# Performance work log

Hardware: AMD Instinct MI355X
Metric: run time of the kernel (lower is better)

The kernel has to match this reference:

```python
import jax, jax.numpy as jnp
import numpy as np

B, L, H, V = 8, 512, 256, 32000
ALPHA = 0.95  # EMA coefficient from __init__
LN_EPS = 1e-5
NORM_EPS = 1e-12  # F.normalize eps


def setup_inputs() -> dict:
    key = jax.random.key(0)
    ks = jax.random.split(key, 8)
    g = lambda k, shape, scale: (jax.random.normal(k, shape, jnp.float32) * scale)
    return {
        "seq": jax.random.randint(ks[0], (B, L), 0, V),
        "embed": g(ks[1], (V, H), 0.02),
        "W1": g(ks[2], (H, 2 * H), 1.0 / np.sqrt(H)),
        "b1": jnp.zeros((2 * H,), jnp.float32),
        "W2": g(ks[3], (2 * H, H), 1.0 / np.sqrt(2 * H)),
        "b2": jnp.zeros((H,), jnp.float32),
        "gamma": jnp.ones((H,), jnp.float32),
        "beta": jnp.zeros((H,), jnp.float32),
        "Wrp": g(ks[4], (H, H), 1.0 / np.sqrt(H)),
        "brp": jnp.zeros((H,), jnp.float32),
        "Wout": g(ks[5], (H, V), 1.0 / np.sqrt(H)),
        "bout": jnp.zeros((V,), jnp.float32),
    }


def _encoder(seq, embed, W1, b1, W2, b2, gamma, beta):
    h = embed[seq]  # [B, L, H]
    ff = jnp.maximum(h @ W1 + b1, 0.0) @ W2 + b2  # Linear-ReLU-Linear
    x = h + ff
    mu = x.mean(-1, keepdims=True)
    var = ((x - mu) ** 2).mean(-1, keepdims=True)
    return (x - mu) / jnp.sqrt(var + LN_EPS) * gamma + beta  # LayerNorm


def reference(seq, embed, W1, b1, W2, b2, gamma, beta, Wrp, brp, Wout, bout):
    h = _encoder(seq, embed, W1, b1, W2, b2, gamma, beta)  # [B, L, H]
    b, l, hd = h.shape
    keys = jnp.swapaxes(h[:, :-1, :], 0, 1)  # time-major [L-1, B, H]

    def step(M, k):
        kn = k / jnp.maximum(jnp.linalg.norm(k, axis=-1, keepdims=True), NORM_EPS)
        dv = k - jnp.einsum('bij,bj->bi', M, kn)  # delta: v - M k_hat
        M = M + (1.0 - ALPHA) * jnp.einsum('bi,bj->bij', dv, kn)  # rank-1 update
        return M, None

    M0 = jnp.zeros((b, hd, hd), h.dtype)
    M, _ = jax.lax.scan(step, M0, keys)  # sequential delta-rule recurrence
    m = jnp.einsum('bij,bj->bi', M, h[:, -1, :])  # read-out with last token
    return (m @ Wrp + brp) @ Wout + bout  # [B, V]
```

## Files before the change

kernel.cpp:

```cpp
#include <hip/hip_runtime.h>

constexpr int Bz  = 8;
constexpr int Lz  = 512;
constexpr int Hz  = 256;
constexpr int H2z = 512;
constexpr int Vz  = 32000;
constexpr int Mz  = Bz * Lz;
constexpr float CF = 0.05f;
constexpr int NB  = 16;

typedef __attribute__((ext_vector_type(8))) short bfrag8;
typedef __attribute__((ext_vector_type(4))) float f32x4v;
typedef __attribute__((ext_vector_type(4))) short s4v;

static __device__ __forceinline__ short f2bf(float f) {
  unsigned u = __builtin_bit_cast(unsigned, f);
  u += 0x7fffu + ((u >> 16) & 1u);
  return (short)(u >> 16);
}

static __device__ __forceinline__ void wcvt_tile(
    const float* __restrict__ src, short* __restrict__ dst,
    int K, int N, int n0, int k0, int tid)
{
  __shared__ float tile[64][68];
  const int rr = tid >> 4, c4 = (tid & 15) << 2;
#pragma unroll
  for (int q = 0; q < 4; ++q) {
    const int kr = rr + q * 16;
    *(float4*)&tile[kr][c4] = *(const float4*)(src + (long)(k0 + kr) * N + n0 + c4);
  }
  __syncthreads();
#pragma unroll
  for (int q = 0; q < 4; ++q) {
    const int nr = rr + q * 16;
    s4v o = { f2bf(tile[c4 + 0][nr]), f2bf(tile[c4 + 1][nr]),
              f2bf(tile[c4 + 2][nr]), f2bf(tile[c4 + 3][nr]) };
    *(s4v*)(dst + (long)(n0 + nr) * K + k0 + c4) = o;
  }
}

__global__ __launch_bounds__(256) void k_wcvt2(
    const float* __restrict__ W1, const float* __restrict__ W2,
    short* __restrict__ Wt1, short* __restrict__ Wt2)
{
  const int bx = blockIdx.x, tid = threadIdx.x;
  if (bx < 32) {
    wcvt_tile(W1, Wt1, Hz, H2z, (bx & 7) * 64, (bx >> 3) * 64, tid);
  } else {
    const int b2 = bx - 32;
    wcvt_tile(W2, Wt2, H2z, Hz, (b2 & 3) * 64, (b2 >> 2) * 64, tid);
  }
}

__global__ __launch_bounds__(256) void k_mfma1(
    const int* __restrict__ seq, const float* __restrict__ embed,
    const short* __restrict__ Wt1, const float* __restrict__ b1,
    short* __restrict__ y1bf)
{
  __shared__ short As[64][32];
  __shared__ short Bs[64][32];
  const int tid = threadIdx.x;
  const int n0 = blockIdx.x * 64, m0 = blockIdx.y * 64;
  const int w = tid >> 6, l = tid & 63;
  const int srow = tid >> 2, skq = (tid & 3) << 3;
  const long abase = (long)seq[m0 + srow] * Hz;
  const f32x4v zero = {0.f, 0.f, 0.f, 0.f};
  f32x4v acc[4] = {zero, zero, zero, zero};
  for (int kc = 0; kc < Hz; kc += 32) {
    const float4 a0 = *(const float4*)(embed + abase + kc + skq);
    const float4 a1 = *(const float4*)(embed + abase + kc + skq + 4);
    const bfrag8 bvl = *(const bfrag8*)(Wt1 + (long)(n0 + srow) * Hz + kc + skq);
    __syncthreads();
    bfrag8 av = { f2bf(a0.x), f2bf(a0.y), f2bf(a0.z), f2bf(a0.w),
                  f2bf(a1.x), f2bf(a1.y), f2bf(a1.z), f2bf(a1.w) };
    *(bfrag8*)&As[srow][skq] = av;
    *(bfrag8*)&Bs[srow][skq] = bvl;
    __syncthreads();
    const bfrag8 a = *(const bfrag8*)&As[(w << 4) + (l & 15)][(l >> 4) << 3];
#pragma unroll
    for (int nn = 0; nn < 4; ++nn) {
      const bfrag8 bb = *(const bfrag8*)&Bs[(nn << 4) + (l & 15)][(l >> 4) << 3];
      acc[nn] = __builtin_amdgcn_mfma_f32_16x16x32_bf16(a, bb, acc[nn], 0, 0, 0);
    }
  }
  const int col0 = l & 15, quad = l >> 4;
#pragma unroll
  for (int nn = 0; nn < 4; ++nn) {
    const int col = n0 + (nn << 4) + col0;
    const float bias = b1[col];
#pragma unroll
    for (int i = 0; i < 4; ++i) {
      const int row = m0 + (w << 4) + (quad << 2) + i;
      y1bf[(long)row * H2z + col] = f2bf(fmaxf(acc[nn][i] + bias, 0.0f));
    }
  }
}

__global__ __launch_bounds__(256) void k_mfma2ln(
    const int* __restrict__ seq, const float* __restrict__ embed,
    const short* __restrict__ y1bf, const short* __restrict__ Wt2,
    const float* __restrict__ b2, const float* __restrict__ gamma,
    const float* __restrict__ beta, float* __restrict__ h,
    float* __restrict__ hn, short* __restrict__ Knb)
{
  __shared__ short As[16][32];
  __shared__ short Bs[256][32];
  __shared__ float red[4][16][2];
  __shared__ float red2[4][16];
  const int tid = threadIdx.x;
  const int m0 = blockIdx.x * 16;
  const int w = tid >> 6, l = tid & 63;
  const int srow = tid >> 2, skq = (tid & 3) << 3;
  const f32x4v zero = {0.f, 0.f, 0.f, 0.f};
  f32x4v acc[4] = {zero, zero, zero, zero};

  for (int kc = 0; kc < H2z; kc += 32) {
    bfrag8 av = {};
    if (tid < 64)
      av = *(const bfrag8*)(y1bf + (long)(m0 + (tid >> 2)) * H2z + kc + skq);
    bfrag8 bv[4];
#pragma unroll
    for (int q = 0; q < 4; ++q)
      bv[q] = *(const bfrag8*)(Wt2 + (long)(srow + (q << 6)) * H2z + kc + skq);
    __syncthreads();
    if (tid < 64) *(bfrag8*)&As[tid >> 2][skq] = av;
#pragma unroll
    for (int q = 0; q < 4; ++q)
      *(bfrag8*)&Bs[srow + (q << 6)][skq] = bv[q];
    __syncthreads();
    const bfrag8 a = *(const bfrag8*)&As[l & 15][(l >> 4) << 3];
#pragma unroll
    for (int nn = 0; nn < 4; ++nn) {
      const bfrag8 bb = *(const bfrag8*)&Bs[(w << 6) + (nn << 4) + (l & 15)][(l >> 4) << 3];
      acc[nn] = __builtin_amdgcn_mfma_f32_16x16x32_bf16(a, bb, acc[nn], 0, 0, 0);
    }
  }

  const int col0 = l & 15, quad = l >> 4;
  float g_r[4], be_r[4], b2_r[4];
#pragma unroll
  for (int nn = 0; nn < 4; ++nn) {
    const int col = (w << 6) + (nn << 4) + col0;
    g_r[nn] = gamma[col]; be_r[nn] = beta[col]; b2_r[nn] = b2[col];
  }

  float v[4][4];
#pragma unroll
  for (int i = 0; i < 4; ++i) {
    const int lr = (quad << 2) + i;
    const int row = m0 + lr;
    const long ebase = (long)seq[row] * Hz;
    float s = 0.0f, ss = 0.0f;
#pragma unroll
    for (int nn = 0; nn < 4; ++nn) {
      const int col = (w << 6) + (nn << 4) + col0;
      const float t = acc[nn][i] + b2_r[nn] + embed[ebase + col];
      v[i][nn] = t; s += t; ss += t * t;
    }
#pragma unroll
    for (int o = 8; o >= 1; o >>= 1) { s += __shfl_xor(s, o); ss += __shfl_xor(ss, o); }
    if ((l & 15) == 0) { red[w][lr][0] = s; red[w][lr][1] = ss; }
  }
  __syncthreads();

#pragma unroll
  for (int i = 0; i < 4; ++i) {
    const int lr = (quad << 2) + i;
    const float s  = red[0][lr][0] + red[1][lr][0] + red[2][lr][0] + red[3][lr][0];
    const float ss = red[0][lr][1] + red[1][lr][1] + red[2][lr][1] + red[3][lr][1];
    const float mu   = s * (1.0f / Hz);
    const float var  = ss * (1.0f / Hz) - mu * mu;
    const float rstd = rsqrtf(var + 1e-5f);
    float hs = 0.0f;
#pragma unroll
    for (int nn = 0; nn < 4; ++nn) {
      const float hv = (v[i][nn] - mu) * rstd * g_r[nn] + be_r[nn];
      v[i][nn] = hv; hs += hv * hv;
    }
#pragma unroll
    for (int o = 8; o >= 1; o >>= 1) hs += __shfl_xor(hs, o);
    if ((l & 15) == 0) red2[w][lr] = hs;
  }
  __syncthreads();

#pragma unroll
  for (int i = 0; i < 4; ++i) {
    const int lr = (quad << 2) + i;
    const float hs = red2[0][lr] + red2[1][lr] + red2[2][lr] + red2[3][lr];
    const float inv = 1.0f / fmaxf(sqrtf(hs), 1e-12f);
    const int row = m0 + lr;
    float* hrow  = h  + (long)row * Hz;
    float* hnrow = hn + (long)row * Hz;
    const int bb_ = row >> 9, t = row & 511;
    short* kr = Knb + ((long)bb_ * 512 + (t < 511 ? 510 - t : 511)) * Hz;
#pragma unroll
    for (int nn = 0; nn < 4; ++nn) {
      const int col = (w << 6) + (nn << 4) + col0;
      const float hv = v[i][nn];
      const float nv = hv * inv;
      hrow[col]  = hv;
      hnrow[col] = nv;
      kr[col] = (t < 511) ? f2bf(nv) : (short)0;
    }
  }
}

__global__ __launch_bounds__(256) void k_gramT(
    const short* __restrict__ Knb, const float* __restrict__ h,
    const float* __restrict__ hn, float* __restrict__ G,
    float* __restrict__ Wsol, float* __restrict__ p)
{
  const int nb = blockIdx.x, mb = blockIdx.y, b = blockIdx.z;
  __shared__ short As[64][32];
  __shared__ short Bs[64][32];
  __shared__ float Gs2[2][32][33];
  __shared__ float qs[Hz];
  if (nb > mb) {
    const int idx = ((nb * (nb - 1)) >> 1) + mb;
    if (idx >= 16) return;
    const int tid = threadIdx.x;
    qs[tid] = h[((long)b * Lz + 511) * Hz + tid];
    __syncthreads();
    const int s = idx * 32 + (tid >> 3);
    const int g = tid & 7;
    float acc = 0.0f;
    if (s <= 510) {
      const float* src = hn + ((long)b * Lz + (510 - s)) * Hz + (g << 5);
#pragma unroll
      for (int q = 0; q < 8; ++q) {
        const float4 vv = *(const float4*)(src + 4 * q);
        const int c = (g << 5) + 4 * q;
        acc += vv.x * qs[c] + vv.y * qs[c + 1] + vv.z * qs[c + 2] + vv.w * qs[c + 3];
      }
    }
#pragma unroll
    for (int o = 4; o >= 1; o >>= 1) acc += __shfl_xor(acc, o);
    if (g == 0) p[(long)b * 512 + s] = acc;
    return;
  }
  const short* Kb = Knb + (long)b * 512 * Hz;
  const int tid = threadIdx.x;
  const int w = tid >> 6, l = tid & 63;
  const int srow = tid >> 2, skq = (tid & 3) << 3;
  const f32x4v zero = {0.f, 0.f, 0.f, 0.f};
  f32x4v acc[4] = {zero, zero, zero, zero};
  for (int kc = 0; kc < Hz; kc += 32) {
    __syncthreads();
    *(bfrag8*)&As[srow][skq] = *(const bfrag8*)(Kb + (long)(mb * 64 + srow) * Hz + kc + skq);
    *(bfrag8*)&Bs[srow][skq] = *(const bfrag8*)(Kb + (long)(nb * 64 + srow) * Hz + kc + skq);
    __syncthreads();
    const bfrag8 a = *(const bfrag8*)&As[(w << 4) + (l & 15)][(l >> 4) << 3];
#pragma unroll
    for (int nn = 0; nn < 4; ++nn) {
      const bfrag8 bb = *(const bfrag8*)&Bs[(nn << 4) + (l & 15)][(l >> 4) << 3];
      acc[nn] = __builtin_amdgcn_mfma_f32_16x16x32_bf16(a, bb, acc[nn], 0, 0, 0);
    }
  }
  const int col0 = l & 15, quad = l >> 4;
  float* Gb = G + (long)b * 512 * 512;
#pragma unroll
  for (int nn = 0; nn < 4; ++nn) {
    const int col = nb * 64 + (nn << 4) + col0;
#pragma unroll
    for (int i = 0; i < 4; ++i) {
      const int row = mb * 64 + (w << 4) + (quad << 2) + i;
      Gb[(long)row * 512 + col] = acc[nn][i];
    }
  }
  if (mb != nb) return;
#pragma unroll
  for (int nn = 0; nn < 4; ++nn) {
    const int lc = (nn << 4) + col0;
#pragma unroll
    for (int i = 0; i < 4; ++i) {
      const int lr = (w << 4) + (quad << 2) + i;
      if ((lr >> 5) == (lc >> 5)) Gs2[lr >> 5][lr & 31][lc & 31] = acc[nn][i];
    }
  }
  __syncthreads();
  if (w < 2 && l < 32) {
    const int c = l;
    float wv[32];
    wv[0] = (c == 0) ? 1.0f : 0.0f;
#pragma unroll
    for (int i = 1; i < 32; ++i) {
      float sum = 0.0f;
#pragma unroll
      for (int j = 0; j < i; ++j) sum = fmaf(Gs2[w][i][j], wv[j], sum);
      wv[i] = ((i == c) ? 1.0f : 0.0f) - CF * sum;
    }
    const int blk = mb * 2 + w;
    float* dst = Wsol + ((long)(b * NB + blk) << 10) + c;
#pragma unroll
    for (int i = 0; i < 32; ++i) dst[i * 32] = wv[i];
  }
}

__global__ __launch_bounds__(256) void k_solve(
    const float* __restrict__ G, const float* __restrict__ p,
    const float* __restrict__ Wsol, float* __restrict__ d_all)
{
  __shared__ float ds[512];
  __shared__ float part[32][9];
  __shared__ float rhs[32];
  const int b = blockIdx.x, tid = threadIdx.x;
  const int i = tid >> 3, g = tid & 7;
  const float* Gb = G + (long)b * 512 * 512;
  const float* pb = p + (long)b * 512;

  for (int blk = 0; blk < NB; ++blk) {
    float acc0 = 0.0f, acc1 = 0.0f;
    const float* grow = Gb + (long)(blk * 32 + i) * 512 + (g << 2);
    int bp = 0;
    for (; bp + 1 < blk; bp += 2) {
      const float4 g0 = *(const float4*)(grow + bp * 32);
      const float4 g1 = *(const float4*)(grow + bp * 32 + 32);
      const int j0 = bp * 32 + (g << 2), j1 = j0 + 32;
      acc0 += g0.x * ds[j0] + g0.y * ds[j0 + 1] + g0.z * ds[j0 + 2] + g0.w * ds[j0 + 3];
      acc1 += g1.x * ds[j1] + g1.y * ds[j1 + 1] + g1.z * ds[j1 + 2] + g1.w * ds[j1 + 3];
    }
    if (bp < blk) {
      const float4 gv = *(const float4*)(grow + bp * 32);
      const int j = bp * 32 + (g << 2);
      acc0 += gv.x * ds[j] + gv.y * ds[j + 1] + gv.z * ds[j + 2] + gv.w * ds[j + 3];
    }
    part[i][g] = acc0 + acc1;
    __syncthreads();
    if (tid < 32) {
      const float c = part[tid][0] + part[tid][1] + part[tid][2] + part[tid][3] +
                      part[tid][4] + part[tid][5] + part[tid][6] + part[tid][7];
      rhs[tid] = pb[blk * 32 + tid] - CF * c;
      const float* wrow = Wsol + ((long)(b * NB + blk) << 10) + tid * 32;
      float dv = 0.0f;
#pragma unroll
      for (int k = 0; k < 32; k += 4) {
        const float4 wv = *(const float4*)(wrow + k);
        dv += wv.x * rhs[k] + wv.y * rhs[k + 1] + wv.z * rhs[k + 2] + wv.w * rhs[k + 3];
      }
      if (blk == NB - 1 && tid == 31) dv = 0.0f;
      ds[blk * 32 + tid] = dv;
      d_all[(long)b * 512 + blk * 32 + tid] = dv;
    }
    __syncthreads();
  }
}

__global__ __launch_bounds__(256) void k_mrp(
    const float* __restrict__ h, const float* __restrict__ d_all,
    float* __restrict__ part)
{
  __shared__ float acc_s[4][Hz];
  const int c = blockIdx.x, b = blockIdx.y, tid = threadIdx.x;
  const int w = tid >> 6, lane = tid & 63;
  const float* hb = h + (long)b * Lz * Hz;
  const float* db = d_all + ((long)b << 9);
  const int t0 = c * 16;
  const int off = lane << 2;
  float4 acc = {0.f, 0.f, 0.f, 0.f};
#pragma unroll
  for (int q = 0; q < 4; ++q) {
    const int t = t0 + (q << 2) + w;
    if (t < 511) {
      const float dv = db[510 - t];
      const float4 hv = *(const float4*)(hb + (long)t * Hz + off);
      acc.x = fmaf(dv, hv.x, acc.x); acc.y = fmaf(dv, hv.y, acc.y);
      acc.z = fmaf(dv, hv.z, acc.z); acc.w = fmaf(dv, hv.w, acc.w);
    }
  }
  *(float4*)&acc_s[w][off] = acc;
  __syncthreads();
  if (tid < Hz) {
    part[((long)b * 32 + c) * Hz + tid] =
        acc_s[0][tid] + acc_s[1][tid] + acc_s[2][tid] + acc_s[3][tid];
  }
}

__global__ __launch_bounds__(256) void k_mr2(
    const float* __restrict__ part, const float* __restrict__ Wrp,
    const float* __restrict__ brp, float* __restrict__ r)
{
  __shared__ float ms[Hz];
  const int b = blockIdx.x, tid = threadIdx.x;
  float acc = 0.0f;
#pragma unroll
  for (int c = 0; c < 32; ++c) acc += part[((long)b * 32 + c) * Hz + tid];
  ms[tid] = CF * acc;
  __syncthreads();
  float racc = 0.0f;
#pragma unroll 8
  for (int e = 0; e < Hz; ++e)
    racc = fmaf(ms[e], Wrp[(long)e * Hz + tid], racc);
  r[b * Hz + tid] = racc + brp[tid];
}

__global__ __launch_bounds__(256) void k_outproj(
    const float* __restrict__ r, const float* __restrict__ Wout,
    const float* __restrict__ bout, float* __restrict__ out)
{
  __shared__ float rs[8 * Hz];
  __shared__ float part[4][8][64];
  const int tid = threadIdx.x, w = tid >> 6, lane = tid & 63;
  ((float4*)rs)[tid * 2 + 0] = ((const float4*)r)[tid * 2 + 0];
  ((float4*)rs)[tid * 2 + 1] = ((const float4*)r)[tid * 2 + 1];
  __syncthreads();
  const int col = blockIdx.x * 64 + lane;
  float acc[8] = {};
  const int i0 = w << 6;
#pragma unroll 8
  for (int ii = 0; ii < 64; ++ii) {
    const int i = i0 + ii;
    const float wv = Wout[(long)i * Vz + col];
#pragma unroll
    for (int bb = 0; bb < 8; ++bb) acc[bb] = fmaf(rs[bb * Hz + i], wv, acc[bb]);
  }
#pragma unroll
  for (int bb = 0; bb < 8; ++bb) part[w][bb][lane] = acc[bb];
  __syncthreads();
  const float bo = bout[col];
  float s0 = part[0][w][lane] + part[1][w][lane] + part[2][w][lane] + part[3][w][lane];
  out[(long)w * Vz + col] = s0 + bo;
  const int w4 = w + 4;
  float s1 = part[0][w4][lane] + part[1][w4][lane] + part[2][w4][lane] + part[3][w4][lane];
  out[(long)w4 * Vz + col] = s1 + bo;
}

extern "C" void kernel_launch(void* const* d_in, const int* in_sizes, int n_in,
                              void* d_out, int out_size, void* d_ws, size_t ws_size,
                              hipStream_t stream)
{
  const int*   seq   = (const int*)  d_in[0];
  const float* embed = (const float*)d_in[1];
  const float* W1    = (const float*)d_in[2];
  const float* b1    = (const float*)d_in[3];
  const float* W2    = (const float*)d_in[4];
  const float* b2    = (const float*)d_in[5];
  const float* gamma = (const float*)d_in[6];
  const float* beta  = (const float*)d_in[7];
  const float* Wrp   = (const float*)d_in[8];
  const float* brp   = (const float*)d_in[9];
  const float* Wout  = (const float*)d_in[10];
  const float* bout  = (const float*)d_in[11];
  float* out = (float*)d_out;

  char* ws = (char*)d_ws;
  const size_t MB = 1024u * 1024u;
  short* y1bf = (short*)(ws);
  float* Gf   = (float*)(ws);
  float* hb   = (float*)(ws + 8 * MB);
  float* hnb  = (float*)(ws + 12 * MB);
  short* Knb  = (short*)(ws + 16 * MB);
  short* Wt1  = (short*)(ws + 18 * MB);
  short* Wt2  = (short*)(ws + 18 * MB + 256 * 1024);
  float* Wsol = (float*)(ws + 18 * MB + 512 * 1024);
  float* pbuf = (float*)(ws + 19 * MB);
  float* dall = (float*)(ws + 19 * MB + 16 * 1024);
  float* prt  = (float*)(ws + 19 * MB + 32 * 1024);
  float* rb   = (float*)(ws + 19 * MB + 288 * 1024);

  k_wcvt2<<<64, 256, 0, stream>>>(W1, W2, Wt1, Wt2);
  k_mfma1<<<dim3(H2z / 64, Mz / 64), 256, 0, stream>>>(seq, embed, Wt1, b1, y1bf);
  k_mfma2ln<<<Mz / 16, 256, 0, stream>>>(seq, embed, y1bf, Wt2, b2, gamma, beta,
                                         hb, hnb, Knb);
  k_gramT<<<dim3(8, 8, Bz), 256, 0, stream>>>(Knb, hb, hnb, Gf, Wsol, pbuf);
  k_solve<<<Bz, 256, 0, stream>>>(Gf, pbuf, Wsol, dall);
  k_mrp<<<dim3(32, Bz), 256, 0, stream>>>(hb, dall, prt);
  k_mr2<<<Bz, 256, 0, stream>>>(prt, Wrp, brp, rb);
  k_outproj<<<Vz / 64, 256, 0, stream>>>(rb, Wout, bout, out);
}
```

Measured before the change: 199.7 us.

## Pre-gather bf16 embeddings and prefetch next block's G/Wsol rows in solve

Gathered embedding rows are converted to bf16 once in the weight-conversion kernel (extra 256 blocks) into a workspace buffer. k_mfma1 then reads those bf16 rows directly instead of re-gathering and converting fp32 embeddings for each of its 8 column blocks. In the sequential k_solve loop, the next block's G row tiles, Wsol rows and p values are loaded into registers before the barrier, hiding global latency on the serial critical path. This costs more registers (gbuf[15], wbuf[8]) and one extra 2 MB buffer write and read.

```diff
diff --git a/kernel.cpp b/kernel.cpp
--- a/kernel.cpp
+++ b/kernel.cpp
@@ -42,21 +42,35 @@
 
 __global__ __launch_bounds__(256) void k_wcvt2(
     const float* __restrict__ W1, const float* __restrict__ W2,
-    short* __restrict__ Wt1, short* __restrict__ Wt2)
+    const int* __restrict__ seq, const float* __restrict__ embed,
+    short* __restrict__ Wt1, short* __restrict__ Wt2, short* __restrict__ Eg)
 {
   const int bx = blockIdx.x, tid = threadIdx.x;
   if (bx < 32) {
     wcvt_tile(W1, Wt1, Hz, H2z, (bx & 7) * 64, (bx >> 3) * 64, tid);
-  } else {
+  } else if (bx < 64) {
     const int b2 = bx - 32;
     wcvt_tile(W2, Wt2, H2z, Hz, (b2 & 3) * 64, (b2 >> 2) * 64, tid);
+  } else {
+    const int row = (bx - 64) * 16 + (tid >> 4);
+    const int c0 = (tid & 15) << 4;
+    const long src = (long)seq[row] * Hz + c0;
+    const float4 v0 = *(const float4*)(embed + src);
+    const float4 v1 = *(const float4*)(embed + src + 4);
+    const float4 v2 = *(const float4*)(embed + src + 8);
+    const float4 v3 = *(const float4*)(embed + src + 12);
+    bfrag8 o0 = { f2bf(v0.x), f2bf(v0.y), f2bf(v0.z), f2bf(v0.w),
+                  f2bf(v1.x), f2bf(v1.y), f2bf(v1.z), f2bf(v1.w) };
+    bfrag8 o1 = { f2bf(v2.x), f2bf(v2.y), f2bf(v2.z), f2bf(v2.w),
+                  f2bf(v3.x), f2bf(v3.y), f2bf(v3.z), f2bf(v3.w) };
+    *(bfrag8*)(Eg + (long)row * Hz + c0) = o0;
+    *(bfrag8*)(Eg + (long)row * Hz + c0 + 8) = o1;
   }
 }
 
 __global__ __launch_bounds__(256) void k_mfma1(
-    const int* __restrict__ seq, const float* __restrict__ embed,
-    const short* __restrict__ Wt1, const float* __restrict__ b1,
-    short* __restrict__ y1bf)
+    const short* __restrict__ Eg, const short* __restrict__ Wt1,
+    const float* __restrict__ b1, short* __restrict__ y1bf)
 {
   __shared__ short As[64][32];
   __shared__ short Bs[64][32];
@@ -64,17 +78,13 @@
   const int n0 = blockIdx.x * 64, m0 = blockIdx.y * 64;
   const int w = tid >> 6, l = tid & 63;
   const int srow = tid >> 2, skq = (tid & 3) << 3;
-  const long abase = (long)seq[m0 + srow] * Hz;
   const f32x4v zero = {0.f, 0.f, 0.f, 0.f};
   f32x4v acc[4] = {zero, zero, zero, zero};
   for (int kc = 0; kc < Hz; kc += 32) {
-    const float4 a0 = *(const float4*)(embed + abase + kc + skq);
-    const float4 a1 = *(const float4*)(embed + abase + kc + skq + 4);
+    const bfrag8 avl = *(const bfrag8*)(Eg + (long)(m0 + srow) * Hz + kc + skq);
     const bfrag8 bvl = *(const bfrag8*)(Wt1 + (long)(n0 + srow) * Hz + kc + skq);
     __syncthreads();
-    bfrag8 av = { f2bf(a0.x), f2bf(a0.y), f2bf(a0.z), f2bf(a0.w),
-                  f2bf(a1.x), f2bf(a1.y), f2bf(a1.z), f2bf(a1.w) };
-    *(bfrag8*)&As[srow][skq] = av;
+    *(bfrag8*)&As[srow][skq] = avl;
     *(bfrag8*)&Bs[srow][skq] = bvl;
     __syncthreads();
     const bfrag8 a = *(const bfrag8*)&As[(w << 4) + (l & 15)][(l >> 4) << 3];
@@ -309,38 +319,55 @@
   const float* Gb = G + (long)b * 512 * 512;
   const float* pb = p + (long)b * 512;
 
+  float4 gbuf[15];
+  float4 wbuf[8];
+  float  pcur = 0.0f;
+  if (tid < 32) {
+#pragma unroll
+    for (int k = 0; k < 8; ++k)
+      wbuf[k] = *(const float4*)(Wsol + ((long)(b * NB) << 10) + tid * 32 + (k << 2));
+    pcur = pb[tid];
+  }
+
   for (int blk = 0; blk < NB; ++blk) {
-    float acc0 = 0.0f, acc1 = 0.0f;
-    const float* grow = Gb + (long)(blk * 32 + i) * 512 + (g << 2);
-    int bp = 0;
-    for (; bp + 1 < blk; bp += 2) {
-      const float4 g0 = *(const float4*)(grow + bp * 32);
-      const float4 g1 = *(const float4*)(grow + bp * 32 + 32);
-      const int j0 = bp * 32 + (g << 2), j1 = j0 + 32;
-      acc0 += g0.x * ds[j0] + g0.y * ds[j0 + 1] + g0.z * ds[j0 + 2] + g0.w * ds[j0 + 3];
-      acc1 += g1.x * ds[j1] + g1.y * ds[j1 + 1] + g1.z * ds[j1 + 2] + g1.w * ds[j1 + 3];
-    }
-    if (bp < blk) {
-      const float4 gv = *(const float4*)(grow + bp * 32);
-      const int j = bp * 32 + (g << 2);
-      acc0 += gv.x * ds[j] + gv.y * ds[j + 1] + gv.z * ds[j + 2] + gv.w * ds[j + 3];
-    }
-    part[i][g] = acc0 + acc1;
+    float acc = 0.0f;
+#pragma unroll
+    for (int bp = 0; bp < 15; ++bp) {
+      if (bp < blk) {
+        const int j = bp * 32 + (g << 2);
+        acc += gbuf[bp].x * ds[j]     + gbuf[bp].y * ds[j + 1] +
+               gbuf[bp].z * ds[j + 2] + gbuf[bp].w * ds[j + 3];
+      }
+    }
+    part[i][g] = acc;
+    if (blk + 1 < NB) {
+      const float* grow = Gb + (long)((blk + 1) * 32 + i) * 512 + (g << 2);
+#pragma unroll
+      for (int bp = 0; bp < 15; ++bp)
+        if (bp <= blk) gbuf[bp] = *(const float4*)(grow + bp * 32);
+    }
     __syncthreads();
     if (tid < 32) {
       const float c = part[tid][0] + part[tid][1] + part[tid][2] + part[tid][3] +
                       part[tid][4] + part[tid][5] + part[tid][6] + part[tid][7];
-      rhs[tid] = pb[blk * 32 + tid] - CF * c;
-      const float* wrow = Wsol + ((long)(b * NB + blk) << 10) + tid * 32;
+      rhs[tid] = pcur - CF * c;
       float dv = 0.0f;
 #pragma unroll
-      for (int k = 0; k < 32; k += 4) {
-        const float4 wv = *(const float4*)(wrow + k);
-        dv += wv.x * rhs[k] + wv.y * rhs[k + 1] + wv.z * rhs[k + 2] + wv.w * rhs[k + 3];
+      for (int k = 0; k < 8; ++k) {
+        const int k0 = k << 2;
+        dv += wbuf[k].x * rhs[k0]     + wbuf[k].y * rhs[k0 + 1] +
+              wbuf[k].z * rhs[k0 + 2] + wbuf[k].w * rhs[k0 + 3];
       }
       if (blk == NB - 1 && tid == 31) dv = 0.0f;
       ds[blk * 32 + tid] = dv;
       d_all[(long)b * 512 + blk * 32 + tid] = dv;
+      if (blk + 1 < NB) {
+#pragma unroll
+        for (int k = 0; k < 8; ++k)
+          wbuf[k] = *(const float4*)(Wsol + ((long)(b * NB + blk + 1) << 10) +
+                                     tid * 32 + (k << 2));
+        pcur = pb[(blk + 1) * 32 + tid];
+      }
     }
     __syncthreads();
   }
@@ -457,9 +484,10 @@
   float* dall = (float*)(ws + 19 * MB + 16 * 1024);
   float* prt  = (float*)(ws + 19 * MB + 32 * 1024);
   float* rb   = (float*)(ws + 19 * MB + 288 * 1024);
-
-  k_wcvt2<<<64, 256, 0, stream>>>(W1, W2, Wt1, Wt2);
-  k_mfma1<<<dim3(H2z / 64, Mz / 64), 256, 0, stream>>>(seq, embed, Wt1, b1, y1bf);
+  short* Eg   = (short*)(ws + 20 * MB);
+
+  k_wcvt2<<<320, 256, 0, stream>>>(W1, W2, seq, embed, Wt1, Wt2, Eg);
+  k_mfma1<<<dim3(H2z / 64, Mz / 64), 256, 0, stream>>>(Eg, Wt1, b1, y1bf);
   k_mfma2ln<<<Mz / 16, 256, 0, stream>>>(seq, embed, y1bf, Wt2, b2, gamma, beta,
                                          hb, hnb, Knb);
   k_gramT<<<dim3(8, 8, Bz), 256, 0, stream>>>(Knb, hb, hnb, Gf, Wsol, pbuf);
```

Result: faster. 177.6 us (-11.1%).
